# Kernel optimization log

Hardware: AMD Instinct MI355X
Metric: run time of the kernel (lower is better)

The kernel has to match this reference:

```python
import jax, jax.numpy as jnp
import numpy as np

EPS = 1e-5

def setup_inputs() -> dict:
    key = jax.random.key(0)
    ks = jax.random.split(key, 6)
    N, M, F, K = 100000, 12, 128, 64
    atom_in_fea = jax.random.normal(ks[0], (N, F), dtype=jnp.float32)
    nbr_fea = jax.random.normal(ks[1], (N, M, K), dtype=jnp.float32)
    nbr_fea_idx = jax.random.randint(ks[2], (N, M), 0, N, dtype=jnp.int64)
    # Linear(2F+K -> 2F): torch stores weight [out, in]
    W = jax.random.normal(ks[3], (2 * F, 2 * F + K), dtype=jnp.float32) * 0.02
    b = jax.random.normal(ks[4], (2 * F,), dtype=jnp.float32) * 0.02
    bn1_gamma = jnp.ones((2 * F,), dtype=jnp.float32)
    bn1_beta = jnp.zeros((2 * F,), dtype=jnp.float32)
    bn2_gamma = jnp.ones((F,), dtype=jnp.float32)
    bn2_beta = jnp.zeros((F,), dtype=jnp.float32)
    return {"atom_in_fea": atom_in_fea, "nbr_fea": nbr_fea, "nbr_fea_idx": nbr_fea_idx,
            "W": W, "b": b, "bn1_gamma": bn1_gamma, "bn1_beta": bn1_beta,
            "bn2_gamma": bn2_gamma, "bn2_beta": bn2_beta}

def _batchnorm(x, gamma, beta):
    # training-mode BatchNorm1d: biased batch variance, eps=1e-5
    mean = jnp.mean(x, axis=0)
    var = jnp.var(x, axis=0)
    return (x - mean) * jax.lax.rsqrt(var + EPS) * gamma + beta

def reference(atom_in_fea, nbr_fea, nbr_fea_idx, W, b, bn1_gamma, bn1_beta, bn2_gamma, bn2_beta):
    N, M = nbr_fea_idx.shape
    F = atom_in_fea.shape[1]
    atom_nbr_fea = atom_in_fea[nbr_fea_idx]                      # [N, M, F] gather
    atom_self = jnp.broadcast_to(atom_in_fea[:, None, :], (N, M, F))
    total = jnp.concatenate([atom_self, atom_nbr_fea, nbr_fea], axis=2)  # [N, M, 2F+K]
    gated = jnp.einsum('nmk,ok->nmo', total, W) + b              # [N, M, 2F]
    gated = _batchnorm(gated.reshape(-1, 2 * F), bn1_gamma, bn1_beta).reshape(N, M, 2 * F)
    nbr_filter, nbr_core = jnp.split(gated, 2, axis=2)
    nbr_sumed = jnp.sum(jax.nn.sigmoid(nbr_filter) * jax.nn.relu(nbr_core), axis=1)  # [N, F]
    nbr_sumed = _batchnorm(nbr_sumed, bn2_gamma, bn2_beta)
    return jax.nn.relu(atom_in_fea + nbr_sumed)
```

## Files before the change

### kernel.cpp

```cpp
#include <hip/hip_runtime.h>

typedef __bf16 bf16x8 __attribute__((ext_vector_type(8)));
typedef __bf16 bf16x4 __attribute__((ext_vector_type(4)));
typedef float  f32x4  __attribute__((ext_vector_type(4)));

#define CIN   320
#define APAD  328
#define BROWS 48

__global__ void detect_kernel(const unsigned short* __restrict__ atom_h,
                              const unsigned* __restrict__ idx_w, int* __restrict__ flags)
{
    if (threadIdx.x == 0 && blockIdx.x == 0) {
        int f32 = 0;
        for (int i = 0; i < 256; ++i) {
            const int e = (atom_h[i] >> 7) & 0xFF;
            if (e >= 134) f32 = 1;
        }
        int i64 = 1;
        for (int i = 0; i < 64; ++i)
            if (idx_w[2 * i + 1] != 0) i64 = 0;
        flags[0] = f32;
        flags[1] = i64;
    }
}

__global__ __launch_bounds__(256) void convert_bf16(const void* __restrict__ src,
    __bf16* __restrict__ dst, long n8, const int* __restrict__ flags)
{
    const long t = (long)blockIdx.x * 256 + threadIdx.x;
    if (t >= n8) return;
    const long i = t * 8;
    if (flags[0]) {
        const float* s = (const float*)src;
        bf16x8 o;
#pragma unroll
        for (int j = 0; j < 8; ++j) o[j] = (__bf16)s[i + j];
        *(bf16x8*)&dst[i] = o;
    } else {
        *(uint4*)&dst[i] = *(const uint4*)((const char*)src + i * 2);
    }
}

template<int MODE>
__global__ __launch_bounds__(256) void gemm_conv(
    const __bf16* __restrict__ atomb, const void* __restrict__ nbrp,
    const void* __restrict__ idxp, const __bf16* __restrict__ Wb,
    const int* __restrict__ flags,
    float* __restrict__ stats1, const float* __restrict__ coef1,
    __bf16* __restrict__ gws, float* __restrict__ nsum)
{
    __shared__ __align__(16) __bf16 Alds[BROWS * APAD];
    __shared__ float sumbuf[512];

    const int tid = threadIdx.x;
    const int blk = blockIdx.x;
    const long rowbase = (long)blk * BROWS;
    const int  n0 = blk * 4;
    const int  isf32 = flags[0];
    const int  isi64 = flags[1];

    if (MODE == 2) { sumbuf[tid] = 0.f; sumbuf[tid + 256] = 0.f; }

    {
        const int c  = tid & 15;
        const int rs = tid >> 4;
#pragma unroll
        for (int it = 0; it < 3; ++it) {
            const int lr = rs + it * 16;
            const int nn = n0 + lr / 12;
            *(uint4*)&Alds[lr * APAD + c * 8] =
                *(const uint4*)&atomb[(long)nn * 128 + c * 8];
            const long r = rowbase + lr;
            const int j = isi64 ? (int)((const long long*)idxp)[r]
                                : ((const int*)idxp)[r];
            *(uint4*)&Alds[lr * APAD + 128 + c * 8] =
                *(const uint4*)&atomb[(long)j * 128 + c * 8];
        }
        if (isf32) {
            const float* nf = (const float*)nbrp;
#pragma unroll
            for (int it = 0; it < 3; ++it) {
                const int lr = rs + it * 16;
                f32x4 v = *(const f32x4*)&nf[(rowbase + lr) * 64 + c * 4];
                bf16x4 o;
#pragma unroll
                for (int j = 0; j < 4; ++j) o[j] = (__bf16)v[j];
                *(bf16x4*)&Alds[lr * APAD + 256 + c * 4] = o;
            }
        } else {
            const __bf16* nb = (const __bf16*)nbrp;
            const int c2  = tid & 7;
            const int rs2 = tid >> 3;
#pragma unroll
            for (int it = 0; it < 2; ++it) {
                const int lr = rs2 + it * 32;
                if (lr < BROWS)
                    *(uint4*)&Alds[lr * APAD + 256 + c2 * 8] =
                        *(const uint4*)&nb[(rowbase + lr) * 64 + c2 * 8];
            }
        }
    }
    __syncthreads();

    const int lane = tid & 63;
    const int wv   = tid >> 6;
    const int quad = lane >> 4;
    const int lrow = lane & 15;
    const int cb0  = wv * 32;

    f32x4 acc[3][4] = {};

    for (int k0 = 0; k0 < CIN; k0 += 32) {
        bf16x8 bfrag[4];
#pragma unroll
        for (int ct = 0; ct < 4; ++ct) {
            const int col = cb0 + ((ct & 1) ? 16 : 0) + ((ct & 2) ? 128 : 0) + lrow;
            bfrag[ct] = *(const bf16x8*)&Wb[col * CIN + k0 + quad * 8];
        }
#pragma unroll
        for (int rt = 0; rt < 3; ++rt) {
            bf16x8 afrag = *(const bf16x8*)&Alds[(rt * 16 + lrow) * APAD + k0 + quad * 8];
#pragma unroll
            for (int ct = 0; ct < 4; ++ct)
                acc[rt][ct] = __builtin_amdgcn_mfma_f32_16x16x32_bf16(
                                  afrag, bfrag[ct], acc[rt][ct], 0, 0, 0);
        }
    }

    if (MODE <= 1) {
        float* st = stats1 + (blk & 63) * 512;
#pragma unroll
        for (int ct = 0; ct < 4; ++ct) {
            float s = 0.f, ss = 0.f;
#pragma unroll
            for (int rt = 0; rt < 3; ++rt)
#pragma unroll
                for (int r = 0; r < 4; ++r) {
                    const float v = acc[rt][ct][r];
                    s += v; ss += v * v;
                }
            s += __shfl_xor(s, 16); ss += __shfl_xor(ss, 16);
            s += __shfl_xor(s, 32); ss += __shfl_xor(ss, 32);
            if (quad == 0) {
                const int col = cb0 + ((ct & 1) ? 16 : 0) + ((ct & 2) ? 128 : 0) + lrow;
                atomicAdd(&st[col], s);
                atomicAdd(&st[256 + col], ss);
            }
        }
        if (MODE == 1) {
#pragma unroll
            for (int rt = 0; rt < 3; ++rt) {
                const long grow = rowbase + rt * 16 + quad * 4;
#pragma unroll
                for (int ct = 0; ct < 4; ++ct) {
                    const int col = cb0 + ((ct & 1) ? 16 : 0) + ((ct & 2) ? 128 : 0) + lrow;
#pragma unroll
                    for (int r = 0; r < 4; ++r)
                        gws[(grow + r) * 256 + col] = (__bf16)acc[rt][ct][r];
                }
            }
        }
    } else {
#pragma unroll
        for (int p = 0; p < 2; ++p) {
            const int cF = cb0 + p * 16 + lrow;
            const float aF = coef1[cF],       bF = coef1[256 + cF];
            const float aC = coef1[128 + cF], bC = coef1[384 + cF];
#pragma unroll
            for (int rt = 0; rt < 3; ++rt)
#pragma unroll
                for (int r = 0; r < 4; ++r) {
                    const float gF = aF * acc[rt][p][r] + bF;
                    const float gC = aC * acc[rt][p + 2][r] + bC;
                    const float val = (1.f / (1.f + __expf(-gF))) * fmaxf(gC, 0.f);
                    const int lr = rt * 16 + quad * 4 + r;
                    atomicAdd(&sumbuf[(lr / 12) * 128 + cF], val);
                }
        }
        __syncthreads();
#pragma unroll
        for (int e = tid; e < 512; e += 256)
            nsum[(long)(n0 + (e >> 7)) * 128 + (e & 127)] = sumbuf[e];
    }
}

__global__ void reduce_bn1(const float* __restrict__ stats1, const void* __restrict__ gamma,
                           const void* __restrict__ beta, float* __restrict__ coef1,
                           const int* __restrict__ flags)
{
    const int c = threadIdx.x;
    const int isf32 = flags[0];
    float s = 0.f, ss = 0.f;
    for (int b = 0; b < 64; ++b) { s += stats1[b * 512 + c]; ss += stats1[b * 512 + 256 + c]; }
    const float inv  = 1.f / 1200000.f;
    const float mean = s * inv;
    const float var  = ss * inv - mean * mean;
    const float g  = isf32 ? ((const float*)gamma)[c] : (float)((const __bf16*)gamma)[c];
    const float bb = isf32 ? ((const float*)beta)[c]  : (float)((const __bf16*)beta)[c];
    const float A = g * rsqrtf(var + 1e-5f);
    coef1[c]       = A;
    coef1[256 + c] = bb - A * mean;
}

__global__ __launch_bounds__(256) void apply_gated(const __bf16* __restrict__ g,
    const float* __restrict__ coef1, float* __restrict__ nsum)
{
    const int tid  = threadIdx.x;
    const int nloc = tid >> 4;
    const int fc   = (tid & 15) * 8;
    const long n   = (long)blockIdx.x * 16 + nloc;
    float aF[8], bF[8], aC[8], bC[8];
#pragma unroll
    for (int j = 0; j < 8; ++j) {
        aF[j] = coef1[fc + j];       bF[j] = coef1[256 + fc + j];
        aC[j] = coef1[128 + fc + j]; bC[j] = coef1[384 + fc + j];
    }
    float s[8] = {};
    const __bf16* base = g + n * (12 * 256);
#pragma unroll
    for (int m = 0; m < 12; ++m) {
        bf16x8 vF = *(const bf16x8*)&base[m * 256 + fc];
        bf16x8 vC = *(const bf16x8*)&base[m * 256 + 128 + fc];
#pragma unroll
        for (int j = 0; j < 8; ++j) {
            const float gF = aF[j] * (float)vF[j] + bF[j];
            const float gC = aC[j] * (float)vC[j] + bC[j];
            s[j] += (1.f / (1.f + __expf(-gF))) * fmaxf(gC, 0.f);
        }
    }
    f32x4 s0 = {s[0], s[1], s[2], s[3]}, s1 = {s[4], s[5], s[6], s[7]};
    *(f32x4*)&nsum[n * 128 + fc]     = s0;
    *(f32x4*)&nsum[n * 128 + fc + 4] = s1;
}

__global__ __launch_bounds__(256) void bn2_stats(const float* __restrict__ nsum,
                                                 float* __restrict__ stats2)
{
    __shared__ float ls[256], lss[256];
    const int tid = threadIdx.x;
    float s = 0.f, ss = 0.f;
    const long stride = (long)gridDim.x * 256;
    for (long i = (long)blockIdx.x * 256 + tid; i < 12800000L; i += stride) {
        const float v = nsum[i]; s += v; ss += v * v;
    }
    ls[tid] = s; lss[tid] = ss;
    __syncthreads();
    if (tid < 128) {
        atomicAdd(&stats2[tid],       ls[tid] + ls[tid + 128]);
        atomicAdd(&stats2[128 + tid], lss[tid] + lss[tid + 128]);
    }
}

__global__ void reduce_bn2(const float* __restrict__ stats2, const void* __restrict__ gamma,
                           const void* __restrict__ beta, float* __restrict__ coef2,
                           const int* __restrict__ flags)
{
    const int c = threadIdx.x;
    const int isf32 = flags[0];
    const float inv  = 1.f / 100000.f;
    const float mean = stats2[c] * inv;
    const float var  = stats2[128 + c] * inv - mean * mean;
    const float g  = isf32 ? ((const float*)gamma)[c] : (float)((const __bf16*)gamma)[c];
    const float bb = isf32 ? ((const float*)beta)[c]  : (float)((const __bf16*)beta)[c];
    const float A = g * rsqrtf(var + 1e-5f);
    coef2[c]       = A;
    coef2[128 + c] = bb - A * mean;
}

__global__ __launch_bounds__(256) void final_out(const __bf16* __restrict__ atomb,
    const float* __restrict__ nsum, const float* __restrict__ coef2,
    void* __restrict__ outp, const int* __restrict__ flags)
{
    const long i = ((long)blockIdx.x * 256 + threadIdx.x) * 8;
    const int f0 = (int)(i & 127);
    bf16x8 a  = *(const bf16x8*)&atomb[i];
    f32x4  u0 = *(const f32x4*)&nsum[i];
    f32x4  u1 = *(const f32x4*)&nsum[i + 4];
    float v[8];
#pragma unroll
    for (int j = 0; j < 8; ++j) {
        const float A  = coef2[f0 + j];
        const float B  = coef2[128 + f0 + j];
        const float ns = (j < 4) ? u0[j] : u1[j - 4];
        v[j] = fmaxf((float)a[j] + A * ns + B, 0.f);
    }
    if (flags[0]) {
        float* o = (float*)outp;
        f32x4 w0 = {v[0], v[1], v[2], v[3]}, w1 = {v[4], v[5], v[6], v[7]};
        *(f32x4*)&o[i]     = w0;
        *(f32x4*)&o[i + 4] = w1;
    } else {
        __bf16* o = (__bf16*)outp;
        bf16x8 w;
#pragma unroll
        for (int j = 0; j < 8; ++j) w[j] = (__bf16)v[j];
        *(bf16x8*)&o[i] = w;
    }
}

extern "C" void kernel_launch(void* const* d_in, const int* in_sizes, int n_in,
                              void* d_out, int out_size, void* d_ws, size_t ws_size,
                              hipStream_t stream)
{
    const void* atom = d_in[0];
    const void* nbr  = d_in[1];
    const void* idxp = d_in[2];
    const void* W    = d_in[3];
    const void* g1   = d_in[5];
    const void* b1   = d_in[6];
    const void* g2   = d_in[7];
    const void* b2   = d_in[8];

    char* ws = (char*)d_ws;
    int*    flags  = (int*)ws;
    float*  stats1 = (float*)(ws + 1024);
    float*  coef1  = (float*)(ws + 132096);
    float*  stats2 = (float*)(ws + 134144);
    float*  coef2  = (float*)(ws + 135168);
    __bf16* atomb  = (__bf16*)(ws + 136192);
    __bf16* Wb     = (__bf16*)(ws + 25736192);
    float*  nsum   = (float*)(ws + 25900032);
    __bf16* gws    = (__bf16*)(ws + 77100032);

    const size_t need_big = 77100032UL + 614400000UL;

    hipMemsetAsync(ws, 0, 136192, stream);
    detect_kernel<<<1, 64, 0, stream>>>((const unsigned short*)atom, (const unsigned*)idxp, flags);
    convert_bf16<<<6250, 256, 0, stream>>>(atom, atomb, 1600000L, flags);
    convert_bf16<<<40, 256, 0, stream>>>(W, Wb, 10240L, flags);

    if (ws_size >= need_big) {
        gemm_conv<1><<<25000, 256, 0, stream>>>(atomb, nbr, idxp, Wb, flags,
                                                stats1, nullptr, gws, nullptr);
        reduce_bn1<<<1, 256, 0, stream>>>(stats1, g1, b1, coef1, flags);
        apply_gated<<<6250, 256, 0, stream>>>(gws, coef1, nsum);
    } else {
        gemm_conv<0><<<25000, 256, 0, stream>>>(atomb, nbr, idxp, Wb, flags,
                                                stats1, nullptr, nullptr, nullptr);
        reduce_bn1<<<1, 256, 0, stream>>>(stats1, g1, b1, coef1, flags);
        gemm_conv<2><<<25000, 256, 0, stream>>>(atomb, nbr, idxp, Wb, flags,
                                                nullptr, coef1, nullptr, nsum);
    }
    bn2_stats<<<512, 256, 0, stream>>>(nsum, stats2);
    reduce_bn2<<<1, 128, 0, stream>>>(stats2, g2, b2, coef2, flags);
    final_out<<<6250, 256, 0, stream>>>(atomb, nsum, coef2, d_out, flags);
}
```

Measured before the change: 1.238 ms.

## Double GEMM row tile, prefetch weight fragments, stage gated stores through LDS

```diff
diff --git a/kernel.cpp b/kernel.cpp
--- a/kernel.cpp
+++ b/kernel.cpp
@@ -6,23 +6,22 @@
 
 #define CIN   320
 #define APAD  328
-#define BROWS 48
+#define ROWS  96
+#define SPAD  264
 
 __global__ void detect_kernel(const unsigned short* __restrict__ atom_h,
                               const unsigned* __restrict__ idx_w, int* __restrict__ flags)
 {
-    if (threadIdx.x == 0 && blockIdx.x == 0) {
-        int f32 = 0;
-        for (int i = 0; i < 256; ++i) {
-            const int e = (atom_h[i] >> 7) & 0xFF;
-            if (e >= 134) f32 = 1;
-        }
-        int i64 = 1;
-        for (int i = 0; i < 64; ++i)
-            if (idx_w[2 * i + 1] != 0) i64 = 0;
-        flags[0] = f32;
-        flags[1] = i64;
-    }
+    const int lane = threadIdx.x;
+    int f32 = 0;
+    for (int i = lane; i < 256; i += 64) {
+        const int e = (atom_h[i] >> 7) & 0xFF;
+        if (e >= 134) f32 = 1;
+    }
+    const unsigned long long m32 = __ballot(f32);
+    const int hi = (idx_w[2 * lane + 1] != 0) ? 1 : 0;
+    const unsigned long long mhi = __ballot(hi);
+    if (lane == 0) { flags[0] = m32 ? 1 : 0; flags[1] = mhi ? 0 : 1; }
 }
 
 __global__ __launch_bounds__(256) void convert_bf16(const void* __restrict__ src,
@@ -43,30 +42,28 @@
 }
 
 template<int MODE>
-__global__ __launch_bounds__(256) void gemm_conv(
+__global__ __launch_bounds__(256, 2) void gemm_conv(
     const __bf16* __restrict__ atomb, const void* __restrict__ nbrp,
     const void* __restrict__ idxp, const __bf16* __restrict__ Wb,
     const int* __restrict__ flags,
     float* __restrict__ stats1, const float* __restrict__ coef1,
     __bf16* __restrict__ gws, float* __restrict__ nsum)
 {
-    __shared__ __align__(16) __bf16 Alds[BROWS * APAD];
-    __shared__ float sumbuf[512];
+    __shared__ __align__(16) char smem[ROWS * APAD * 2];
+    __bf16* Alds = (__bf16*)smem;
 
     const int tid = threadIdx.x;
     const int blk = blockIdx.x;
-    const long rowbase = (long)blk * BROWS;
-    const int  n0 = blk * 4;
+    const long rowbase = (long)blk * ROWS;
+    const int  n0 = blk * 8;
     const int  isf32 = flags[0];
     const int  isi64 = flags[1];
-
-    if (MODE == 2) { sumbuf[tid] = 0.f; sumbuf[tid + 256] = 0.f; }
 
     {
         const int c  = tid & 15;
         const int rs = tid >> 4;
 #pragma unroll
-        for (int it = 0; it < 3; ++it) {
+        for (int it = 0; it < 6; ++it) {
             const int lr = rs + it * 16;
             const int nn = n0 + lr / 12;
             *(uint4*)&Alds[lr * APAD + c * 8] =
@@ -80,7 +77,7 @@
         if (isf32) {
             const float* nf = (const float*)nbrp;
 #pragma unroll
-            for (int it = 0; it < 3; ++it) {
+            for (int it = 0; it < 6; ++it) {
                 const int lr = rs + it * 16;
                 f32x4 v = *(const f32x4*)&nf[(rowbase + lr) * 64 + c * 4];
                 bf16x4 o;
@@ -93,11 +90,10 @@
             const int c2  = tid & 7;
             const int rs2 = tid >> 3;
 #pragma unroll
-            for (int it = 0; it < 2; ++it) {
+            for (int it = 0; it < 3; ++it) {
                 const int lr = rs2 + it * 32;
-                if (lr < BROWS)
-                    *(uint4*)&Alds[lr * APAD + 256 + c2 * 8] =
-                        *(const uint4*)&nb[(rowbase + lr) * 64 + c2 * 8];
+                *(uint4*)&Alds[lr * APAD + 256 + c2 * 8] =
+                    *(const uint4*)&nb[(rowbase + lr) * 64 + c2 * 8];
             }
         }
     }
@@ -109,22 +105,38 @@
     const int lrow = lane & 15;
     const int cb0  = wv * 32;
 
-    f32x4 acc[3][4] = {};
-
-    for (int k0 = 0; k0 < CIN; k0 += 32) {
-        bf16x8 bfrag[4];
-#pragma unroll
-        for (int ct = 0; ct < 4; ++ct) {
-            const int col = cb0 + ((ct & 1) ? 16 : 0) + ((ct & 2) ? 128 : 0) + lrow;
-            bfrag[ct] = *(const bf16x8*)&Wb[col * CIN + k0 + quad * 8];
-        }
-#pragma unroll
-        for (int rt = 0; rt < 3; ++rt) {
+    int cols[4];
+    const __bf16* wp[4];
+#pragma unroll
+    for (int ct = 0; ct < 4; ++ct) {
+        cols[ct] = cb0 + ((ct & 1) ? 16 : 0) + ((ct & 2) ? 128 : 0) + lrow;
+        wp[ct] = Wb + (long)cols[ct] * CIN + quad * 8;
+    }
+
+    f32x4 acc[6][4] = {};
+    bf16x8 bcur[4], bnxt[4];
+#pragma unroll
+    for (int ct = 0; ct < 4; ++ct) bcur[ct] = *(const bf16x8*)(wp[ct]);
+
+#pragma unroll
+    for (int kk = 0; kk < 10; ++kk) {
+        const int k0 = kk * 32;
+        if (kk < 9) {
+#pragma unroll
+            for (int ct = 0; ct < 4; ++ct)
+                bnxt[ct] = *(const bf16x8*)(wp[ct] + k0 + 32);
+        }
+#pragma unroll
+        for (int rt = 0; rt < 6; ++rt) {
             bf16x8 afrag = *(const bf16x8*)&Alds[(rt * 16 + lrow) * APAD + k0 + quad * 8];
 #pragma unroll
             for (int ct = 0; ct < 4; ++ct)
                 acc[rt][ct] = __builtin_amdgcn_mfma_f32_16x16x32_bf16(
-                                  afrag, bfrag[ct], acc[rt][ct], 0, 0, 0);
+                                  afrag, bcur[ct], acc[rt][ct], 0, 0, 0);
+        }
+        if (kk < 9) {
+#pragma unroll
+            for (int ct = 0; ct < 4; ++ct) bcur[ct] = bnxt[ct];
         }
     }
 
@@ -134,7 +146,7 @@
         for (int ct = 0; ct < 4; ++ct) {
             float s = 0.f, ss = 0.f;
 #pragma unroll
-            for (int rt = 0; rt < 3; ++rt)
+            for (int rt = 0; rt < 6; ++rt)
 #pragma unroll
                 for (int r = 0; r < 4; ++r) {
                     const float v = acc[rt][ct][r];
@@ -143,32 +155,42 @@
             s += __shfl_xor(s, 16); ss += __shfl_xor(ss, 16);
             s += __shfl_xor(s, 32); ss += __shfl_xor(ss, 32);
             if (quad == 0) {
-                const int col = cb0 + ((ct & 1) ? 16 : 0) + ((ct & 2) ? 128 : 0) + lrow;
-                atomicAdd(&st[col], s);
-                atomicAdd(&st[256 + col], ss);
+                atomicAdd(&st[cols[ct]], s);
+                atomicAdd(&st[256 + cols[ct]], ss);
             }
         }
         if (MODE == 1) {
-#pragma unroll
-            for (int rt = 0; rt < 3; ++rt) {
-                const long grow = rowbase + rt * 16 + quad * 4;
-#pragma unroll
-                for (int ct = 0; ct < 4; ++ct) {
-                    const int col = cb0 + ((ct & 1) ? 16 : 0) + ((ct & 2) ? 128 : 0) + lrow;
+            __syncthreads();
+            __bf16* S = (__bf16*)smem;
+#pragma unroll
+            for (int rt = 0; rt < 6; ++rt)
+#pragma unroll
+                for (int ct = 0; ct < 4; ++ct)
 #pragma unroll
                     for (int r = 0; r < 4; ++r)
-                        gws[(grow + r) * 256 + col] = (__bf16)acc[rt][ct][r];
-                }
+                        S[(rt * 16 + quad * 4 + r) * SPAD + cols[ct]] = (__bf16)acc[rt][ct][r];
+            __syncthreads();
+            const __bf16* Sr = (const __bf16*)smem;
+            __bf16* dst = gws + rowbase * 256;
+#pragma unroll
+            for (int it = 0; it < 12; ++it) {
+                const int e = tid * 8 + it * 2048;
+                *(bf16x8*)&dst[e] = *(const bf16x8*)&Sr[(e >> 8) * SPAD + (e & 255)];
             }
         }
     } else {
+        __syncthreads();
+        float* sumbuf = (float*)smem;
+#pragma unroll
+        for (int e = tid; e < 1024; e += 256) sumbuf[e] = 0.f;
+        __syncthreads();
 #pragma unroll
         for (int p = 0; p < 2; ++p) {
             const int cF = cb0 + p * 16 + lrow;
             const float aF = coef1[cF],       bF = coef1[256 + cF];
             const float aC = coef1[128 + cF], bC = coef1[384 + cF];
 #pragma unroll
-            for (int rt = 0; rt < 3; ++rt)
+            for (int rt = 0; rt < 6; ++rt)
 #pragma unroll
                 for (int r = 0; r < 4; ++r) {
                     const float gF = aF * acc[rt][p][r] + bF;
@@ -180,7 +202,7 @@
         }
         __syncthreads();
 #pragma unroll
-        for (int e = tid; e < 512; e += 256)
+        for (int e = tid; e < 1024; e += 256)
             nsum[(long)(n0 + (e >> 7)) * 128 + (e & 127)] = sumbuf[e];
     }
 }
@@ -331,15 +353,15 @@
     convert_bf16<<<40, 256, 0, stream>>>(W, Wb, 10240L, flags);
 
     if (ws_size >= need_big) {
-        gemm_conv<1><<<25000, 256, 0, stream>>>(atomb, nbr, idxp, Wb, flags,
+        gemm_conv<1><<<12500, 256, 0, stream>>>(atomb, nbr, idxp, Wb, flags,
                                                 stats1, nullptr, gws, nullptr);
         reduce_bn1<<<1, 256, 0, stream>>>(stats1, g1, b1, coef1, flags);
         apply_gated<<<6250, 256, 0, stream>>>(gws, coef1, nsum);
     } else {
-        gemm_conv<0><<<25000, 256, 0, stream>>>(atomb, nbr, idxp, Wb, flags,
+        gemm_conv<0><<<12500, 256, 0, stream>>>(atomb, nbr, idxp, Wb, flags,
                                                 stats1, nullptr, nullptr, nullptr);
         reduce_bn1<<<1, 256, 0, stream>>>(stats1, g1, b1, coef1, flags);
-        gemm_conv<2><<<25000, 256, 0, stream>>>(atomb, nbr, idxp, Wb, flags,
+        gemm_conv<2><<<12500, 256, 0, stream>>>(atomb, nbr, idxp, Wb, flags,
                                                 nullptr, coef1, nullptr, nsum);
     }
     bn2_stats<<<512, 256, 0, stream>>>(nsum, stats2);
```

Result: faster. 1.065 ms (-14.0%).
